# Kernel tuning notes

Measured on AMD Instinct MI355X. Metric: run time of the kernel, lower is better.

Reference implementation:

```python
import jax, jax.numpy as jnp
import numpy as np

B, DIM, HEADS, H, W, WS, AWS = 8, 64, 4, 256, 256, 8, 8
HD = DIM // HEADS
SCALE = HD ** -0.5


def _grid_sample_zeros(img, grid):
    # img: (N, C, Hi, Wi); grid: (N, Ho, Wo, 2) with (x, y) in [-1, 1]
    # bilinear, align_corners=True, zero padding (matches F.grid_sample)
    N, C, Hi, Wi = img.shape
    gx = (grid[..., 0] + 1.0) * 0.5 * (Wi - 1)
    gy = (grid[..., 1] + 1.0) * 0.5 * (Hi - 1)
    x0 = jnp.floor(gx).astype(jnp.int32); x1 = x0 + 1
    y0 = jnp.floor(gy).astype(jnp.int32); y1 = y0 + 1
    wx1 = gx - x0; wx0 = 1.0 - wx1
    wy1 = gy - y0; wy0 = 1.0 - wy1

    def one(im, x0, x1, y0, y1, wx0, wx1, wy0, wy1):
        def g(yi, xi):
            valid = ((yi >= 0) & (yi < Hi) & (xi >= 0) & (xi < Wi)).astype(im.dtype)
            v = im[:, jnp.clip(yi, 0, Hi - 1), jnp.clip(xi, 0, Wi - 1)]
            return v * valid[None]
        return (g(y0, x0) * (wy0 * wx0)[None] + g(y0, x1) * (wy0 * wx1)[None]
                + g(y1, x0) * (wy1 * wx0)[None] + g(y1, x1) * (wy1 * wx1)[None])

    return jax.vmap(one)(img, x0, x1, y0, y1, wx0, wx1, wy0, wy1)


def _rel_index():
    c = np.stack(np.meshgrid(np.arange(AWS), np.arange(AWS), indexing='ij'))
    cf = c.reshape(2, -1)
    rel = (cf[:, :, None] - cf[:, None, :]).transpose(1, 2, 0).copy()
    rel[:, :, 0] += AWS - 1
    rel[:, :, 1] += AWS - 1
    rel[:, :, 0] *= 2 * AWS - 1
    return rel.sum(-1)  # (AWS*AWS, AWS*AWS)


_REL_IDX = jnp.asarray(_rel_index())


def setup_inputs():
    key = jax.random.key(0)
    ks = jax.random.split(key, 8)
    s = 0.02
    return {
        'x': jax.random.normal(ks[0], (B, DIM, H, W), jnp.float32),
        'qkv_w': jax.random.normal(ks[1], (3 * DIM, DIM), jnp.float32) * s,
        'qkv_b': jnp.zeros((3 * DIM,), jnp.float32),
        'proj_w': jax.random.normal(ks[2], (DIM, DIM), jnp.float32) * s,
        'proj_b': jnp.zeros((DIM,), jnp.float32),
        'off_w': jax.random.normal(ks[3], (2 * HEADS, DIM), jnp.float32) * s,
        'off_b': jnp.zeros((2 * HEADS,), jnp.float32),
        'sc_w': jax.random.normal(ks[4], (2 * HEADS, DIM), jnp.float32) * s,
        'sc_b': jnp.zeros((2 * HEADS,), jnp.float32),
        'rel_bias': jax.random.normal(ks[5], ((WS + AWS - 1) ** 2, HEADS), jnp.float32) * s,
    }


def reference(x, qkv_w, qkv_b, proj_w, proj_b, off_w, off_b, sc_w, sc_b, rel_bias):
    b, dim, h, w = x.shape
    pad_td = (WS - h % WS) % WS; pad_lr = (WS - w % WS) % WS
    pt, pd = pad_td // 2, pad_td - pad_td // 2
    pl, pr = pad_lr // 2, pad_lr - pad_lr // 2
    eh, ew = h + pad_td, w + pad_lr
    wnh, wnw = eh // WS, ew // WS

    # per-pixel reference grid in [-1,1]; channel 0 = x(w-axis), channel 1 = y(h-axis)
    ref_h = jnp.linspace(-1.0, 1.0, eh)
    ref_w = jnp.linspace(-1.0, 1.0, ew)
    base = jnp.stack([jnp.broadcast_to(ref_w[None, :], (eh, ew)),
                      jnp.broadcast_to(ref_h[:, None], (eh, ew))], 0)
    base = base.reshape(2, wnh, WS, wnw, WS)

    # zero-mean window-relative attention coordinates
    bch = jnp.arange(AWS, dtype=jnp.float32) * 2 * WS / AWS / (eh - 1); bch = bch - bch.mean()
    bcw = jnp.arange(AWS, dtype=jnp.float32) * 2 * WS / AWS / (ew - 1); bcw = bcw - bcw.mean()
    ech = jnp.tile(bch, wnh)
    ecw = jnp.tile(bcw, wnw)
    wc = jnp.stack([jnp.broadcast_to(ecw[None, :], (wnh * AWS, wnw * AWS)),
                    jnp.broadcast_to(ech[:, None], (wnh * AWS, wnw * AWS))], 0)
    wc = wc.reshape(2, wnh, AWS, wnw, AWS)

    xp = jnp.pad(x, ((0, 0), (0, 0), (pt, pd), (pl, pr)))

    # offsets / scales: avgpool(WS) -> leaky_relu -> 1x1 conv
    pooled = xp.reshape(b, dim, wnh, WS, wnw, WS).mean(axis=(3, 5))
    act = jax.nn.leaky_relu(pooled, 0.01)
    off = jnp.einsum('bchw,oc->bohw', act, off_w) + off_b[None, :, None, None]
    off = off.reshape(b * HEADS, 2, wnh, wnw)
    off = off * jnp.array([1.0 / (h // WS), 1.0 / (w // WS)], off.dtype)[None, :, None, None]
    sc = jnp.einsum('bchw,oc->bohw', act, sc_w) + sc_b[None, :, None, None]
    sc = sc.reshape(b * HEADS, 2, wnh, wnw)

    coords = (base[None] + wc[None] * sc[:, :, :, None, :, None]
              + off[:, :, :, None, :, None])  # (b*heads, 2, wnh, AWS, wnw, AWS)
    grid = coords.transpose(0, 2, 3, 4, 5, 1).reshape(b * HEADS, wnh * AWS, wnw * AWS, 2)

    # qkv 1x1 conv, then spatial pad
    qkv = jnp.einsum('bchw,oc->bohw', x, qkv_w) + qkv_b[None, :, None, None]
    qkv = qkv.reshape(b, 3, HEADS, HD, h, w)
    qkv = jnp.pad(qkv, ((0, 0),) * 4 + ((pt, pd), (pl, pr)))
    q = qkv[:, 0].reshape(b * HEADS, HD, eh, ew)
    k = qkv[:, 1].reshape(b * HEADS, HD, eh, ew)
    v = qkv[:, 2].reshape(b * HEADS, HD, eh, ew)

    k_sel = _grid_sample_zeros(k, grid)
    v_sel = _grid_sample_zeros(v, grid)

    q = q.reshape(b, HEADS, HD, wnh, WS, wnw, WS).transpose(0, 3, 5, 1, 4, 6, 2)
    q = q.reshape(b * wnh * wnw, HEADS, WS * WS, HD)

    def to_win(t):
        t = t.reshape(b, HEADS, HD, wnh, AWS, wnw, AWS).transpose(0, 3, 5, 1, 4, 6, 2)
        return t.reshape(b * wnh * wnw, HEADS, AWS * AWS, HD)

    kw, vw = to_win(k_sel), to_win(v_sel)

    dots = jnp.einsum('wnqd,wnkd->wnqk', q, kw) * SCALE
    bias = rel_bias[_REL_IDX]  # (WS*WS, AWS*AWS, HEADS)
    dots = dots + bias.transpose(2, 0, 1)[None]
    attn = jax.nn.softmax(dots, axis=-1)
    out = jnp.einsum('wnqk,wnkd->wnqd', attn, vw)

    out = out.reshape(b, wnh, wnw, HEADS, WS, WS, HD).transpose(0, 3, 6, 1, 4, 2, 5)
    out = out.reshape(b, dim, eh, ew)[:, :, pt:h + pt, pl:w + pl]
    out = jnp.einsum('bchw,oc->bohw', out, proj_w) + proj_b[None, :, None, None]
    return out
```

## Files before the change

### kernel.cpp

```cpp
#include <hip/hip_runtime.h>

#define BATCH 8
#define CDIM 64
#define NHEADS 4
#define HD 16
#define IMG 256
#define WSZ 8
#define WN 32
#define NWIN (WN * WN)

static constexpr size_t OFFSC_FLOATS = (size_t)BATCH * NHEADS * NWIN * 4;
static constexpr size_t MAP_ELEMS = (size_t)BATCH * NHEADS * IMG * IMG * HD;
static constexpr size_t ACTG_BYTES = (size_t)BATCH * CDIM * WN * WN * 4;

typedef unsigned short u16;
typedef __attribute__((ext_vector_type(2))) _Float16 h2;
typedef __attribute__((ext_vector_type(8))) _Float16 h8;
typedef __attribute__((ext_vector_type(4))) float f32x4;

__device__ __forceinline__ unsigned cvt_pk_f16(float a, float b) {
    unsigned r;
    asm("v_cvt_pkrtz_f16_f32 %0, %1, %2" : "=v"(r) : "v"(a), "v"(b));
    return r;
}
__device__ __forceinline__ float rcpf(float s) {
    float r;
    asm("v_rcp_f32 %0, %1" : "=v"(r) : "v"(s));
    return r;
}
union UH2 { unsigned u; h2 h; };
__device__ __forceinline__ h2 u2h2(unsigned u) { UH2 x; x.u = u; return x.h; }
__device__ __forceinline__ unsigned h22u(h2 h) { UH2 x; x.h = h; return x.u; }
__device__ __forceinline__ u16 f2h(float f) {
    _Float16 h = (_Float16)f;
    u16 r;
    __builtin_memcpy(&r, &h, 2);
    return r;
}
__device__ __forceinline__ unsigned pk_rne(float a, float b) {
    return (unsigned)f2h(a) | ((unsigned)f2h(b) << 16);
}

__global__ __launch_bounds__(256) void k_offmv(const float* __restrict__ actg,
                                               const float* __restrict__ off_w,
                                               const float* __restrict__ off_b,
                                               const float* __restrict__ sc_w,
                                               const float* __restrict__ sc_b,
                                               float* __restrict__ offsc) {
    __shared__ float act[CDIM][WN + 1];
    int b = blockIdx.x >> 5, wh = blockIdx.x & 31;
    int t = threadIdx.x;
    for (int i = t; i < CDIM * WN; i += 256) {
        int c = i >> 5, ww = i & 31;
        float v = actg[(((size_t)b * CDIM + c) * WN + wh) * WN + ww] * (1.0f / 64.0f);
        act[c][ww] = (v >= 0.f) ? v : 0.01f * v;
    }
    __syncthreads();
    int ww = t >> 3, oi = t & 7;
    float ao = off_b[oi], as = sc_b[oi];
    #pragma unroll 8
    for (int c = 0; c < CDIM; c++) {
        float av = act[c][ww];
        ao += av * off_w[oi * CDIM + c];
        as += av * sc_w[oi * CDIM + c];
    }
    ao *= (1.0f / 32.0f);
    int n = oi >> 1, d = oi & 1;
    size_t base = (((size_t)(b * NHEADS + n) * NWIN) + wh * WN + ww) << 2;
    offsc[base + d] = ao;
    offsc[base + 2 + d] = as;
}

__global__ __launch_bounds__(256) void k_wconv(const float* __restrict__ qkv_w,
                                               const float* __restrict__ proj_w,
                                               unsigned* __restrict__ wbf) {
    int i = blockIdx.x * 256 + threadIdx.x;
    if (i < 6144) {
        wbf[i] = cvt_pk_f16(qkv_w[2 * i], qkv_w[2 * i + 1]);
    } else if (i < 8192) {
        int j = i - 6144;
        wbf[i] = cvt_pk_f16(proj_w[2 * j], proj_w[2 * j + 1]);
    }
}

__global__ __launch_bounds__(256) void k_qkv_mfma(const float* __restrict__ x,
                                                  const u16* __restrict__ wbf,
                                                  const float* __restrict__ qkv_b,
                                                  u16* __restrict__ qm,
                                                  u16* __restrict__ km,
                                                  u16* __restrict__ vm,
                                                  float* __restrict__ actg) {
    __shared__ u16 Alds[256 * 64];

    int bid = blockIdx.x;
    bid = (bid & 7) * 256 + (bid >> 3);
    int b = bid >> 8, y = bid & 255;
    int t = threadIdx.x;

    {
        const float* xp = x + ((size_t)b * CDIM * IMG + y) * IMG + t;
        u16* row = Alds + t * 64;
        int sw = t & 7;
        int wh = y >> 3, ww = t >> 3;
        float* ap = actg + (((size_t)b * CDIM) * WN + wh) * WN + ww;
        bool lead = (t & 7) == 0;
        #pragma unroll
        for (int cp = 0; cp < 32; cp++) {
            float a = xp[(size_t)(2 * cp) * IMG * IMG];
            float bq = xp[(size_t)(2 * cp + 1) * IMG * IMG];
            float sa = a, sb = bq;
            #pragma unroll
            for (int s = 1; s < 8; s <<= 1) {
                sa += __shfl_xor(sa, s, 64);
                sb += __shfl_xor(sb, s, 64);
            }
            if (lead) {
                atomicAdd(ap + (size_t)(2 * cp) * (WN * WN), sa);
                atomicAdd(ap + (size_t)(2 * cp + 1) * (WN * WN), sb);
            }
            unsigned pk = cvt_pk_f16(a, bq);
            int c = 2 * cp;
            int chunk = c >> 3;
            *(unsigned*)(row + ((chunk ^ sw) << 3) + (c & 7)) = pk;
        }
    }

    int wv = t >> 6, l = t & 63;
    int lr = l & 15, lg = l >> 4;

    h8 afr[4][2];
    #pragma unroll
    for (int pg = 0; pg < 4; pg++) {
        int p = wv * 64 + pg * 16 + lr;
        const u16* prow = Alds + p * 64;
        int psw = p & 7;
        #pragma unroll
        for (int kb = 0; kb < 2; kb++) {
            int chunk = kb * 4 + lg;
            afr[pg][kb] = *(const h8*)(prow + ((chunk ^ psw) << 3));
        }
    }

    u16* const maps[3] = { qm, km, vm };
    #pragma unroll
    for (int ot = 0; ot < 12; ot++) {
        int o = ot * 16 + lr;
        float4 b4 = *(const float4*)(qkv_b + ot * 16 + lg * 4);
        h8 bfr0 = *(const h8*)(wbf + o * 64 + lg * 8);
        h8 bfr1 = *(const h8*)(wbf + o * 64 + 32 + lg * 8);

        f32x4 acc[4];
        #pragma unroll
        for (int pg = 0; pg < 4; pg++) {
            acc[pg] = (f32x4){ b4.x, b4.y, b4.z, b4.w };
            acc[pg] = __builtin_amdgcn_mfma_f32_16x16x32_f16(bfr0, afr[pg][0], acc[pg], 0, 0, 0);
            acc[pg] = __builtin_amdgcn_mfma_f32_16x16x32_f16(bfr1, afr[pg][1], acc[pg], 0, 0, 0);
        }

        u16* mp = maps[ot >> 2];
        int n = ot & 3;
        size_t base = ((size_t)(b * NHEADS + n) * IMG * IMG + (size_t)y * IMG) * HD;
        #pragma unroll
        for (int pg = 0; pg < 4; pg++) {
            size_t sb = base + (size_t)(wv * 64 + pg * 16 + lr) * HD + lg * 4;
            *(uint2*)(mp + sb) = make_uint2(pk_rne(acc[pg][0], acc[pg][1]),
                                            pk_rne(acc[pg][2], acc[pg][3]));
        }
    }
}

__global__ __launch_bounds__(256, 2) void k_attn3(const u16* __restrict__ qm,
                                                  const u16* __restrict__ km,
                                                  const u16* __restrict__ vm,
                                                  const u16* __restrict__ wproj,
                                                  const float* __restrict__ proj_b,
                                                  const float* __restrict__ rel_bias,
                                                  const float* __restrict__ offsc,
                                                  float* __restrict__ out) {
    __shared__ float biasS[NHEADS * 225];
    __shared__ _Float16 hb[NHEADS][2048];
    _Float16* Ob = &hb[0][0];

    int blk = blockIdx.x;
    blk = (blk & 7) * 1024 + (blk >> 3);
    int b = blk >> 10, wh = (blk >> 5) & 31, ww = blk & 31;
    int tid = threadIdx.x, n = tid >> 6, l = tid & 63;
    int g = l >> 4, cl = l & 15;
    int y0 = wh * WSZ, x0 = ww * WSZ;
    const h8 z8 = {};

    for (int i = tid; i < NHEADS * 225; i += 256) {
        int hn = i / 225, idx = i - hn * 225;
        biasS[i] = rel_bias[idx * NHEADS + hn] * 4.0f;
    }

    float4 os4 = *(const float4*)(offsc + ((((size_t)(b * NHEADS + n) * NWIN) + wh * WN + ww) << 2));

    h8 qfr[4];
    {
        const u16* qb = qm + ((size_t)(b * NHEADS + n) << 16) * HD;
        #pragma unroll
        for (int qt = 0; qt < 4; qt++) {
            int q = qt * 16 + cl;
            qfr[qt] = (g < 2)
                ? *(const h8*)(qb + ((size_t)(y0 + (q >> 3)) * IMG + (x0 + (q & 7))) * HD + g * 8)
                : z8;
        }
    }

    h8 wfr[2];
    #pragma unroll
    for (int h = 0; h < 2; h++)
        wfr[h] = *(const h8*)(wproj + (n * 16 + cl) * 64 + h * 32 + g * 8);
    float4 pb4 = *(const float4*)(proj_b + n * 16 + g * 4);

    {
        float offx = os4.x, offy = os4.y;
        float scx = os4.z, scy = os4.w;
        int pi = l >> 3, pj = l & 7;
        float gx = (float)(x0 + pj) + ((float)(2 * pj - 7) * (1.0f / 255.0f) * scx + offx) * 127.5f;
        float gy = (float)(y0 + pi) + ((float)(2 * pi - 7) * (1.0f / 255.0f) * scy + offy) * 127.5f;

        float fx0 = floorf(gx), fy0 = floorf(gy);
        int ix0 = (int)fx0, iy0 = (int)fy0;
        float wx1 = gx - fx0, wx0 = 1.f - wx1;
        float wy1 = gy - fy0, wy0 = 1.f - wy1;

        const u16* kb = km + ((size_t)(b * NHEADS + n) << 16) * HD;
        const u16* vb = vm + ((size_t)(b * NHEADS + n) << 16) * HD;

        int iys[2] = { iy0, iy0 + 1 };
        int ixs[2] = { ix0, ix0 + 1 };
        float wys[2] = { wy0, wy1 };
        float wxs[2] = { wx0, wx1 };

        size_t offs[4];
        h2 w2[4];
        #pragma unroll
        for (int t = 0; t < 4; t++) {
            int yy = iys[t >> 1], xq = ixs[t & 1];
            float wgt = wys[t >> 1] * wxs[t & 1];
            if (yy < 0 || yy >= IMG || xq < 0 || xq >= IMG) wgt = 0.f;
            int yc = min(max(yy, 0), IMG - 1), xc = min(max(xq, 0), IMG - 1);
            offs[t] = ((size_t)yc * IMG + xc) * HD;
            _Float16 hw = (_Float16)wgt;
            w2[t] = (h2){ hw, hw };
        }

        h2 kacc[8], vacc[8];
        #pragma unroll
        for (int i = 0; i < 8; i++) {
            kacc[i] = (h2){ (_Float16)0, (_Float16)0 };
            vacc[i] = (h2){ (_Float16)0, (_Float16)0 };
        }

        {
            uint4 t0[4], t1[4];
            #pragma unroll
            for (int t = 0; t < 4; t++) {
                const uint4* p = (const uint4*)(kb + offs[t]);
                t0[t] = p[0]; t1[t] = p[1];
            }
            #pragma unroll
            for (int t = 0; t < 4; t++) {
                kacc[0] += w2[t] * u2h2(t0[t].x); kacc[1] += w2[t] * u2h2(t0[t].y);
                kacc[2] += w2[t] * u2h2(t0[t].z); kacc[3] += w2[t] * u2h2(t0[t].w);
                kacc[4] += w2[t] * u2h2(t1[t].x); kacc[5] += w2[t] * u2h2(t1[t].y);
                kacc[6] += w2[t] * u2h2(t1[t].z); kacc[7] += w2[t] * u2h2(t1[t].w);
            }
        }
        {
            uint4 t0[4], t1[4];
            #pragma unroll
            for (int t = 0; t < 4; t++) {
                const uint4* p = (const uint4*)(vb + offs[t]);
                t0[t] = p[0]; t1[t] = p[1];
            }
            #pragma unroll
            for (int t = 0; t < 4; t++) {
                vacc[0] += w2[t] * u2h2(t0[t].x); vacc[1] += w2[t] * u2h2(t0[t].y);
                vacc[2] += w2[t] * u2h2(t0[t].z); vacc[3] += w2[t] * u2h2(t0[t].w);
                vacc[4] += w2[t] * u2h2(t1[t].x); vacc[5] += w2[t] * u2h2(t1[t].y);
                vacc[6] += w2[t] * u2h2(t1[t].z); vacc[7] += w2[t] * u2h2(t1[t].w);
            }
        }

        uint4* kp = (uint4*)(&hb[n][0] + (size_t)l * 16);
        kp[0] = make_uint4(h22u(kacc[0]), h22u(kacc[1]), h22u(kacc[2]), h22u(kacc[3]));
        kp[1] = make_uint4(h22u(kacc[4]), h22u(kacc[5]), h22u(kacc[6]), h22u(kacc[7]));

        int p = cl * 4 + g;
        #pragma unroll
        for (int i = 0; i < 8; i++) {
            int d0 = 2 * i, d1 = 2 * i + 1;
            hb[n][1024 + d0 * 64 + (p ^ ((d0 & 3) << 4))] = vacc[i][0];
            hb[n][1024 + d1 * 64 + (p ^ ((d1 & 3) << 4))] = vacc[i][1];
        }
    }

    h8 kfr[4], vfr[2];
    #pragma unroll
    for (int kt = 0; kt < 4; kt++)
        kfr[kt] = (g < 2) ? *(const h8*)(&hb[n][0] + (kt * 16 + cl) * 16 + g * 8) : z8;
    #pragma unroll
    for (int h = 0; h < 2; h++)
        vfr[h] = *(const h8*)(&hb[n][1024] + cl * 64 + ((h * 32 + g * 8) ^ ((cl & 3) << 4)));

    __syncthreads();

    f32x4 dacc[4][4];
    #pragma unroll
    for (int qt = 0; qt < 4; qt++) {
        #pragma unroll
        for (int kt = 0; kt < 4; kt++) {
            int pik = kt * 2 + (cl >> 3), pjk = cl & 7;
            int bidx = n * 225 + (7 - pik) * 15 + (7 - pjk) + (qt * 2 + (g >> 1)) * 15 + (g & 1) * 4;
            f32x4 c = { biasS[bidx], biasS[bidx + 1], biasS[bidx + 2], biasS[bidx + 3] };
            dacc[qt][kt] = __builtin_amdgcn_mfma_f32_16x16x32_f16(qfr[qt], kfr[kt], c, 0, 0, 0);
        }
    }

    _Float16* Pb = &hb[n][0];
    f32x4 oacc[4];
    float inv_[4][4];
    #pragma unroll
    for (int qt = 0; qt < 4; qt++) {
        #pragma unroll
        for (int kt = 0; kt < 4; kt++)
            #pragma unroll
            for (int r = 0; r < 4; r++)
                dacc[qt][kt][r] = exp2f(dacc[qt][kt][r] * 0.36067376f);
        #pragma unroll
        for (int r = 0; r < 4; r++) {
            float s0 = dacc[qt][0][r] + dacc[qt][1][r] + dacc[qt][2][r] + dacc[qt][3][r];
            #pragma unroll
            for (int s = 1; s < 16; s <<= 1) s0 += __shfl_xor(s0, s, 64);
            inv_[qt][r] = rcpf(s0);
        }
        #pragma unroll
        for (int r = 0; r < 4; r++) {
            unsigned lo = cvt_pk_f16(dacc[qt][0][r], dacc[qt][1][r]);
            unsigned hi = cvt_pk_f16(dacc[qt][2][r], dacc[qt][3][r]);
            *(uint2*)((u16*)Pb + (g * 4 + r) * 64 + ((cl * 4) ^ (r << 4))) = make_uint2(lo, hi);
        }
        f32x4 pv = { 0.f, 0.f, 0.f, 0.f };
        #pragma unroll
        for (int h = 0; h < 2; h++) {
            h8 af = *(const h8*)(Pb + cl * 64 + ((h * 32 + g * 8) ^ ((cl & 3) << 4)));
            pv = __builtin_amdgcn_mfma_f32_16x16x32_f16(af, vfr[h], pv, 0, 0, 0);
        }
        oacc[qt] = pv;
    }

    __syncthreads();

    #pragma unroll
    for (int qt = 0; qt < 4; qt++)
        #pragma unroll
        for (int r = 0; r < 4; r++) {
            int q = qt * 16 + g * 4 + r;
            Ob[q * 64 + ((n * 16 + cl) ^ (g << 4))] = (_Float16)(oacc[qt][r] * inv_[qt][r]);
        }
    __syncthreads();

    #pragma unroll
    for (int qt = 0; qt < 4; qt++) {
        f32x4 pa = { pb4.x, pb4.y, pb4.z, pb4.w };
        #pragma unroll
        for (int h = 0; h < 2; h++) {
            h8 of = *(const h8*)(Ob + (qt * 16 + cl) * 64 + ((h * 32 + g * 8) ^ ((cl >> 2) << 4)));
            pa = __builtin_amdgcn_mfma_f32_16x16x32_f16(wfr[h], of, pa, 0, 0, 0);
        }
        int q = qt * 16 + cl;
        #pragma unroll
        for (int r = 0; r < 4; r++) {
            out[((size_t)(b * CDIM + n * 16 + g * 4 + r) * IMG + y0 + (q >> 3)) * IMG + x0 + (q & 7)] = pa[r];
        }
    }
}

extern "C" void kernel_launch(void* const* d_in, const int* in_sizes, int n_in,
                              void* d_out, int out_size, void* d_ws, size_t ws_size,
                              hipStream_t stream) {
    const float* x      = (const float*)d_in[0];
    const float* qkv_w  = (const float*)d_in[1];
    const float* qkv_b  = (const float*)d_in[2];
    const float* proj_w = (const float*)d_in[3];
    const float* proj_b = (const float*)d_in[4];
    const float* off_w  = (const float*)d_in[5];
    const float* off_b  = (const float*)d_in[6];
    const float* sc_w   = (const float*)d_in[7];
    const float* sc_b   = (const float*)d_in[8];
    const float* rel_b  = (const float*)d_in[9];
    float* out = (float*)d_out;

    float* ws = (float*)d_ws;
    float* offsc = ws;
    u16* wqkv = (u16*)(ws + OFFSC_FLOATS);
    u16* wprj = wqkv + 12288;
    u16* qmm = wprj + 4096;
    u16* kmm = qmm + MAP_ELEMS;
    u16* vmm = kmm + MAP_ELEMS;
    float* actg = out;

    hipMemsetAsync(actg, 0, ACTG_BYTES, stream);
    k_wconv<<<32, 256, 0, stream>>>(qkv_w, proj_w, (unsigned*)wqkv);
    k_qkv_mfma<<<BATCH * IMG, 256, 0, stream>>>(x, wqkv, qkv_b, qmm, kmm, vmm, actg);
    k_offmv<<<BATCH * WN, 256, 0, stream>>>(actg, off_w, off_b, sc_w, sc_b, offsc);
    k_attn3<<<BATCH * NWIN, 256, 0, stream>>>(qmm, kmm, vmm, wprj, proj_b,
                                              rel_b, offsc, out);
}
```

Measured before the change: 234.1 us.

## Fold softmax scale into Q, use DPP row sums and LDS-based window pooling

The softmax scale and log2(e) factor are folded into Q when it is stored, and the bias is premultiplied by log2(e). This lets the attention kernel call the raw exp2 builtin with no per-element multiply. The 16-lane softmax row sum now uses DPP row rotations instead of cross-lane shuffles. Window-mean pooling in the QKV kernel no longer does shuffles per channel; after a barrier it reads the fp16 tile back from LDS, sums in packed fp16 and issues the atomics. The costs are an extra block barrier and lower-precision fp16 pooling sums.

```diff
diff --git a/kernel.cpp b/kernel.cpp
--- a/kernel.cpp
+++ b/kernel.cpp
@@ -18,6 +18,9 @@
 typedef __attribute__((ext_vector_type(8))) _Float16 h8;
 typedef __attribute__((ext_vector_type(4))) float f32x4;
 
+#define QSCALE 0.36067376f
+#define L2E    1.4426950f
+
 __device__ __forceinline__ unsigned cvt_pk_f16(float a, float b) {
     unsigned r;
     asm("v_cvt_pkrtz_f16_f32 %0, %1, %2" : "=v"(r) : "v"(a), "v"(b));
@@ -39,6 +42,22 @@
 }
 __device__ __forceinline__ unsigned pk_rne(float a, float b) {
     return (unsigned)f2h(a) | ((unsigned)f2h(b) << 16);
+}
+
+#define DPP_RADD(x, ctrl)                                                         \
+    x += __int_as_float(__builtin_amdgcn_update_dpp(                              \
+        0, __float_as_int(x), (ctrl), 0xF, 0xF, false))
+
+__global__ __launch_bounds__(256) void k_wconv(const float* __restrict__ qkv_w,
+                                               const float* __restrict__ proj_w,
+                                               unsigned* __restrict__ wbf) {
+    int i = blockIdx.x * 256 + threadIdx.x;
+    if (i < 6144) {
+        wbf[i] = cvt_pk_f16(qkv_w[2 * i], qkv_w[2 * i + 1]);
+    } else if (i < 8192) {
+        int j = i - 6144;
+        wbf[i] = cvt_pk_f16(proj_w[2 * j], proj_w[2 * j + 1]);
+    }
 }
 
 __global__ __launch_bounds__(256) void k_offmv(const float* __restrict__ actg,
@@ -71,18 +90,6 @@
     offsc[base + 2 + d] = as;
 }
 
-__global__ __launch_bounds__(256) void k_wconv(const float* __restrict__ qkv_w,
-                                               const float* __restrict__ proj_w,
-                                               unsigned* __restrict__ wbf) {
-    int i = blockIdx.x * 256 + threadIdx.x;
-    if (i < 6144) {
-        wbf[i] = cvt_pk_f16(qkv_w[2 * i], qkv_w[2 * i + 1]);
-    } else if (i < 8192) {
-        int j = i - 6144;
-        wbf[i] = cvt_pk_f16(proj_w[2 * j], proj_w[2 * j + 1]);
-    }
-}
-
 __global__ __launch_bounds__(256) void k_qkv_mfma(const float* __restrict__ x,
                                                   const u16* __restrict__ wbf,
                                                   const float* __restrict__ qkv_b,
@@ -101,27 +108,36 @@
         const float* xp = x + ((size_t)b * CDIM * IMG + y) * IMG + t;
         u16* row = Alds + t * 64;
         int sw = t & 7;
-        int wh = y >> 3, ww = t >> 3;
-        float* ap = actg + (((size_t)b * CDIM) * WN + wh) * WN + ww;
-        bool lead = (t & 7) == 0;
         #pragma unroll
         for (int cp = 0; cp < 32; cp++) {
             float a = xp[(size_t)(2 * cp) * IMG * IMG];
             float bq = xp[(size_t)(2 * cp + 1) * IMG * IMG];
-            float sa = a, sb = bq;
-            #pragma unroll
-            for (int s = 1; s < 8; s <<= 1) {
-                sa += __shfl_xor(sa, s, 64);
-                sb += __shfl_xor(sb, s, 64);
-            }
-            if (lead) {
-                atomicAdd(ap + (size_t)(2 * cp) * (WN * WN), sa);
-                atomicAdd(ap + (size_t)(2 * cp + 1) * (WN * WN), sb);
-            }
             unsigned pk = cvt_pk_f16(a, bq);
             int c = 2 * cp;
             int chunk = c >> 3;
             *(unsigned*)(row + ((chunk ^ sw) << 3) + (c & 7)) = pk;
+        }
+    }
+    __syncthreads();
+
+    {
+        int cp = t & 31;
+        int chunk = cp >> 2;
+        int coff = (2 * cp) & 7;
+        int wh = y >> 3;
+        float* ap = actg + (((size_t)b * CDIM + 2 * cp) * WN + wh) * WN;
+        #pragma unroll
+        for (int k = 0; k < 4; k++) {
+            int ww = ((t >> 5) << 2) + k;
+            h2 s2 = {};
+            #pragma unroll
+            for (int px8 = 0; px8 < 8; px8++) {
+                int px = ww * 8 + px8;
+                unsigned v = *(const unsigned*)(Alds + px * 64 + ((chunk ^ (px & 7)) << 3) + coff);
+                s2 += u2h2(v);
+            }
+            atomicAdd(ap + ww, (float)s2[0]);
+            atomicAdd(ap + (size_t)(WN * WN) + ww, (float)s2[1]);
         }
     }
 
@@ -163,8 +179,14 @@
         #pragma unroll
         for (int pg = 0; pg < 4; pg++) {
             size_t sb = base + (size_t)(wv * 64 + pg * 16 + lr) * HD + lg * 4;
-            *(uint2*)(mp + sb) = make_uint2(pk_rne(acc[pg][0], acc[pg][1]),
-                                            pk_rne(acc[pg][2], acc[pg][3]));
+            if (ot < 4) {
+                *(uint2*)(mp + sb) = make_uint2(
+                    pk_rne(acc[pg][0] * QSCALE, acc[pg][1] * QSCALE),
+                    pk_rne(acc[pg][2] * QSCALE, acc[pg][3] * QSCALE));
+            } else {
+                *(uint2*)(mp + sb) = make_uint2(pk_rne(acc[pg][0], acc[pg][1]),
+                                                pk_rne(acc[pg][2], acc[pg][3]));
+            }
         }
     }
 }
@@ -191,7 +213,7 @@
 
     for (int i = tid; i < NHEADS * 225; i += 256) {
         int hn = i / 225, idx = i - hn * 225;
-        biasS[i] = rel_bias[idx * NHEADS + hn] * 4.0f;
+        biasS[i] = rel_bias[idx * NHEADS + hn] * L2E;
     }
 
     float4 os4 = *(const float4*)(offsc + ((((size_t)(b * NHEADS + n) * NWIN) + wh * WN + ww) << 2));
@@ -329,12 +351,14 @@
         for (int kt = 0; kt < 4; kt++)
             #pragma unroll
             for (int r = 0; r < 4; r++)
-                dacc[qt][kt][r] = exp2f(dacc[qt][kt][r] * 0.36067376f);
+                dacc[qt][kt][r] = __builtin_amdgcn_exp2f(dacc[qt][kt][r]);
         #pragma unroll
         for (int r = 0; r < 4; r++) {
-            float s0 = dacc[qt][0][r] + dacc[qt][1][r] + dacc[qt][2][r] + dacc[qt][3][r];
-            #pragma unroll
-            for (int s = 1; s < 16; s <<= 1) s0 += __shfl_xor(s0, s, 64);
+            float s0 = (dacc[qt][0][r] + dacc[qt][1][r]) + (dacc[qt][2][r] + dacc[qt][3][r]);
+            DPP_RADD(s0, 0x121);
+            DPP_RADD(s0, 0x122);
+            DPP_RADD(s0, 0x124);
+            DPP_RADD(s0, 0x128);
             inv_[qt][r] = rcpf(s0);
         }
         #pragma unroll
```

Result: slower. 252.7 us (+7.9%).
